# Optimization experiments

Hardware: AMD Instinct MI355X
Metric: run time of the kernel (lower is better)

## Reference

```python
import jax, jax.numpy as jnp
import numpy as np

N_NODES = 50000
N_EDGES = 800000
NUM_GRAPHS = 512
IN_DIM = 128
HID = 128
OUT_DIM = 1


def setup_inputs() -> dict:
    key = jax.random.key(0)
    ks = jax.random.split(key, 8)
    x = jax.random.normal(ks[0], (N_NODES, IN_DIM), dtype=jnp.float32)
    edge_index = jax.random.randint(ks[1], (2, N_EDGES), 0, N_NODES, dtype=jnp.int64)
    batch = jnp.sort(jax.random.randint(ks[2], (N_NODES,), 0, NUM_GRAPHS, dtype=jnp.int64))
    s1 = 1.0 / np.sqrt(IN_DIM)
    s2 = 1.0 / np.sqrt(HID)
    W1 = jax.random.normal(ks[3], (IN_DIM, HID), dtype=jnp.float32) * s1
    b1 = jnp.zeros((HID,), dtype=jnp.float32)
    W2 = jax.random.normal(ks[4], (HID, HID), dtype=jnp.float32) * s2
    b2 = jnp.zeros((HID,), dtype=jnp.float32)
    Wl = jax.random.normal(ks[5], (HID, OUT_DIM), dtype=jnp.float32) * s2
    bl = jnp.zeros((OUT_DIM,), dtype=jnp.float32)
    return {"x": x, "edge_index": edge_index, "batch": batch,
            "W1": W1, "b1": b1, "W2": W2, "b2": b2, "Wl": Wl, "bl": bl}


def _gcn_conv(x, src, dst, norm, W, b):
    # GCNConv: D^{-1/2}(A+I)D^{-1/2} X W + b (self-loops already in src/dst)
    h = x @ W                                    # [N, H]
    msg = h[src] * norm[:, None]                 # gather + edge-normalize
    agg = jax.ops.segment_sum(msg, dst, num_segments=N_NODES)  # scatter-add
    return agg + b


def reference(x, edge_index, batch, W1, b1, W2, b2, Wl, bl):
    loops = jnp.arange(N_NODES, dtype=edge_index.dtype)
    src = jnp.concatenate([edge_index[0], loops])
    dst = jnp.concatenate([edge_index[1], loops])
    deg = jax.ops.segment_sum(jnp.ones_like(dst, dtype=x.dtype), dst, num_segments=N_NODES)
    dinv = jax.lax.rsqrt(deg)                    # deg >= 1 due to self-loops
    norm = dinv[src] * dinv[dst]                 # symmetric normalization per edge

    h = jax.nn.relu(_gcn_conv(x, src, dst, norm, W1, b1))
    h = jax.nn.relu(_gcn_conv(h, src, dst, norm, W2, b2))

    # global_mean_pool over graph ids
    sums = jax.ops.segment_sum(h, batch, num_segments=NUM_GRAPHS)
    cnts = jax.ops.segment_sum(jnp.ones((N_NODES,), dtype=h.dtype), batch, num_segments=NUM_GRAPHS)
    pooled = sums / jnp.maximum(cnts, 1.0)[:, None]

    out = jax.nn.sigmoid(pooled @ Wl + bl)       # [G, 1]
    return out.squeeze(1)                        # [G]
```

## Files before the change

### kernel.cpp

```cpp
#include <hip/hip_runtime.h>
#include <hip/hip_bf16.h>

#define N_NODES 50000
#define N_EDGES 800000
#define NUM_GRAPHS 512
#define MAXDEG 64
#define EPB 4096
#define P1_BLOCKS 196
#define NBUCK 256
#define NPB 196

typedef short short8 __attribute__((ext_vector_type(8)));
typedef unsigned short u16x8 __attribute__((ext_vector_type(8)));
typedef float f32x4 __attribute__((ext_vector_type(4)));

__device__ __forceinline__ unsigned short f2bu(float f) {
    __hip_bfloat16 h = __float2bfloat16(f);
    return *reinterpret_cast<unsigned short*>(&h);
}
__device__ __forceinline__ float bu2f(unsigned short u) {
    unsigned int v = ((unsigned int)u) << 16;
    float f;
    __builtin_memcpy(&f, &v, 4);
    return f;
}

__global__ __launch_bounds__(256) void bin_k(const int* __restrict__ ei,
                                             unsigned int* __restrict__ staging,
                                             int* __restrict__ cnts_tbl,
                                             int* __restrict__ offs_tbl,
                                             unsigned short* __restrict__ hs1,
                                             unsigned short* __restrict__ hs2) {
    __shared__ unsigned int st[EPB];
    __shared__ int cnt[NBUCK], cur[NBUCK], scan[NBUCK];
    int b = blockIdx.x, t = threadIdx.x;
    if (b == 0 && t < 64)
        ((unsigned int*)(hs1 + (size_t)N_NODES * 128))[t] = 0u;
    if (b == 1 && t < 64)
        ((unsigned int*)(hs2 + (size_t)N_NODES * 128))[t] = 0u;
    cnt[t] = 0;
    __syncthreads();

    int e0 = b * EPB;
    int srcv[16], dstv[16], bk[16];
#pragma unroll
    for (int k = 0; k < 16; ++k) {
        int e = e0 + k * 256 + t;
        bool ok = e < N_EDGES;
        srcv[k] = ok ? ei[e] : 0;
        dstv[k] = ok ? ei[N_EDGES + e] : 0;
        bk[k] = ok ? (dstv[k] / NPB) : -1;
        if (ok) atomicAdd(&cnt[bk[k]], 1);
    }
    __syncthreads();
    scan[t] = cnt[t];
    __syncthreads();
    for (int off = 1; off < 256; off <<= 1) {
        int u = t >= off ? scan[t - off] : 0;
        __syncthreads();
        scan[t] += u;
        __syncthreads();
    }
    int excl = scan[t] - cnt[t];
    cur[t] = excl;
    cnts_tbl[t * P1_BLOCKS + b] = cnt[t];
    offs_tbl[t * P1_BLOCKS + b] = excl;
    __syncthreads();
#pragma unroll
    for (int k = 0; k < 16; ++k) {
        if (bk[k] >= 0) {
            int pos = atomicAdd(&cur[bk[k]], 1);
            int dl = dstv[k] - bk[k] * NPB;
            st[pos] = (unsigned int)srcv[k] | ((unsigned int)dl << 16);
        }
    }
    __syncthreads();
    unsigned int* gout = staging + (size_t)b * EPB;
    for (int i = t; i < EPB; i += 256) gout[i] = st[i];
}

__global__ __launch_bounds__(256) void adjbuild_k(const unsigned int* __restrict__ staging,
                                                  const int* __restrict__ cnts_tbl,
                                                  const int* __restrict__ offs_tbl,
                                                  unsigned short* __restrict__ adj,
                                                  int* __restrict__ cnt,
                                                  float* __restrict__ dinv,
                                                  const float* __restrict__ W1,
                                                  const float* __restrict__ W2,
                                                  unsigned short* __restrict__ W1t,
                                                  unsigned short* __restrict__ W2t) {
    int b = blockIdx.x, t = threadIdx.x;
    if (b >= NBUCK) {
        int wb = b - NBUCK;
        const float* W = wb < 64 ? W1 : W2;
        unsigned short* Wt = wb < 64 ? W1t : W2t;
        int idx = (wb & 63) * 256 + t;
        int k = idx >> 7, n = idx & 127;
        Wt[n * 128 + k] = f2bu(W[idx]);
        return;
    }
    __shared__ unsigned short adjL[NPB * MAXDEG];
    __shared__ int cntL[NPB];
    __shared__ int segStart[P1_BLOCKS + 1];
    __shared__ int segOff[P1_BLOCKS];
    __shared__ int tmp[256];

    if (t < NPB) cntL[t] = 0;
    int c = t < P1_BLOCKS ? cnts_tbl[b * P1_BLOCKS + t] : 0;
    if (t < P1_BLOCKS) segOff[t] = offs_tbl[b * P1_BLOCKS + t];
    tmp[t] = c;
    __syncthreads();
    for (int off = 1; off < 256; off <<= 1) {
        int u = t >= off ? tmp[t - off] : 0;
        __syncthreads();
        tmp[t] += u;
        __syncthreads();
    }
    if (t < P1_BLOCKS) segStart[t] = tmp[t] - c;
    if (t == 0) segStart[P1_BLOCKS] = tmp[P1_BLOCKS - 1];
    __syncthreads();

    int T = segStart[P1_BLOCKS];
    for (int f = t; f < T; f += 256) {
        int lo = 0, hi = P1_BLOCKS;
        while (hi - lo > 1) {
            int m = (lo + hi) >> 1;
            if (segStart[m] <= f) lo = m; else hi = m;
        }
        unsigned int p = staging[(size_t)lo * EPB + segOff[lo] + (f - segStart[lo])];
        int src = p & 0xFFFF;
        int dl = p >> 16;
        int slot = atomicAdd(&cntL[dl], 1);
        if (slot < MAXDEG - 1) adjL[dl * MAXDEG + slot] = (unsigned short)src;
    }
    __syncthreads();

    int nodeBase = b * NPB;
    if (t < NPB) {
        int node = nodeBase + t;
        int cc = cntL[t];
        int ec = cc < MAXDEG - 1 ? cc : MAXDEG - 1;
        adjL[t * MAXDEG + ec] = (unsigned short)node;
        int tot = ec + 1, tot4 = (tot + 3) & ~3;
        for (int s = tot; s < tot4; ++s) adjL[t * MAXDEG + s] = (unsigned short)N_NODES;
        if (node < N_NODES) {
            cnt[node] = cc;
            dinv[node] = rsqrtf((float)cc + 1.0f);
        }
    }
    __syncthreads();
    unsigned int* g = (unsigned int*)(adj + (size_t)nodeBase * MAXDEG);
    const unsigned int* l = (const unsigned int*)adjL;
    for (int i = t; i < NPB * MAXDEG / 2; i += 256) g[i] = l[i];
}

__global__ __launch_bounds__(256) void gemm_k(const float* __restrict__ Ap,
                                              const unsigned short* __restrict__ Wt,
                                              const float* __restrict__ dinv,
                                              unsigned short* __restrict__ C) {
    __shared__ unsigned short Wl[128 * 136];
    int t = threadIdx.x;
    for (int idx = t; idx < 2048; idx += 256) {
        int n = idx >> 4, c = idx & 15;
        *(u16x8*)(Wl + n * 136 + c * 8) = *(const u16x8*)(Wt + n * 128 + c * 8);
    }
    __syncthreads();

    int wave = t >> 6, lane = t & 63, quad = lane >> 4, ln = lane & 15;
    int rb = blockIdx.x * 128 + wave * 16;

    short8 a[2][4];
#pragma unroll
    for (int mt = 0; mt < 2; ++mt) {
        int r = rb + mt * 64 + ln;
        r = r < N_NODES ? r : N_NODES - 1;
        const float* arow = Ap + (size_t)r * 128 + quad * 8;
#pragma unroll
        for (int ks = 0; ks < 4; ++ks) {
            float4 v0 = *(const float4*)(arow + ks * 32);
            float4 v1 = *(const float4*)(arow + ks * 32 + 4);
            short8 av;
            av[0] = (short)f2bu(v0.x); av[1] = (short)f2bu(v0.y);
            av[2] = (short)f2bu(v0.z); av[3] = (short)f2bu(v0.w);
            av[4] = (short)f2bu(v1.x); av[5] = (short)f2bu(v1.y);
            av[6] = (short)f2bu(v1.z); av[7] = (short)f2bu(v1.w);
            a[mt][ks] = av;
        }
    }

    f32x4 acc[2][8];
#pragma unroll
    for (int mt = 0; mt < 2; ++mt)
#pragma unroll
        for (int ct = 0; ct < 8; ++ct) acc[mt][ct] = (f32x4){0.f, 0.f, 0.f, 0.f};

#pragma unroll
    for (int ks = 0; ks < 4; ++ks)
#pragma unroll
        for (int ct = 0; ct < 8; ++ct) {
            short8 b = *(const short8*)(Wl + (ct * 16 + ln) * 136 + ks * 32 + quad * 8);
            acc[0][ct] = __builtin_amdgcn_mfma_f32_16x16x32_bf16(a[0][ks], b, acc[0][ct], 0, 0, 0);
            acc[1][ct] = __builtin_amdgcn_mfma_f32_16x16x32_bf16(a[1][ks], b, acc[1][ct], 0, 0, 0);
        }

#pragma unroll
    for (int mt = 0; mt < 2; ++mt) {
#pragma unroll
        for (int rr = 0; rr < 4; ++rr) {
            int r = rb + mt * 64 + quad * 4 + rr;
            if (r >= N_NODES) continue;
            float dv = dinv[r];
#pragma unroll
            for (int ct = 0; ct < 8; ++ct)
                C[(size_t)r * 128 + ct * 16 + ln] = f2bu(acc[mt][ct][rr] * dv);
        }
    }
}

__global__ __launch_bounds__(256) void agg_gemm_k(const unsigned short* __restrict__ hs1,
                                                  const unsigned short* __restrict__ adj,
                                                  const int* __restrict__ cnt,
                                                  const float* __restrict__ dinv,
                                                  const float* __restrict__ bias,
                                                  const unsigned short* __restrict__ W2t,
                                                  unsigned short* __restrict__ hs2) {
    __shared__ unsigned short Wl[128 * 136];
    __shared__ unsigned short h1t[16 * 136];
    int t = threadIdx.x, wave = t >> 6, lane = t & 63;
    int quad = lane >> 4, fl = lane & 15;
    for (int idx = t; idx < 2048; idx += 256) {
        int n = idx >> 4, c = idx & 15;
        *(u16x8*)(Wl + n * 136 + c * 8) = *(const u16x8*)(W2t + n * 128 + c * 8);
    }
    int nb = blockIdx.x * 16;

    float4 b0 = *(const float4*)(bias + fl * 8);
    float4 b1f = *(const float4*)(bias + fl * 8 + 4);

#pragma unroll
    for (int q = 0; q < 4; ++q) {
        int lr = wave * 4 + q;
        int node = nb + lr;
        int idxv = (int)adj[node * MAXDEG + lane];
        int c = cnt[node];
        int ec = c < MAXDEG - 1 ? c : MAXDEG - 1;
        int iters = (ec + 4) >> 2;

        float acc[8];
#pragma unroll
        for (int j = 0; j < 8; ++j) acc[j] = 0.f;

        int i = 0;
        for (; i + 2 <= iters; i += 2) {
            int s0 = __shfl(idxv, i * 4 + quad, 64);
            int s1 = __shfl(idxv, i * 4 + 4 + quad, 64);
            u16x8 v0 = *(const u16x8*)(hs1 + (size_t)s0 * 128 + fl * 8);
            u16x8 v1 = *(const u16x8*)(hs1 + (size_t)s1 * 128 + fl * 8);
#pragma unroll
            for (int j = 0; j < 8; ++j) acc[j] += bu2f(v0[j]) + bu2f(v1[j]);
        }
        if (i < iters) {
            int s0 = __shfl(idxv, i * 4 + quad, 64);
            u16x8 v0 = *(const u16x8*)(hs1 + (size_t)s0 * 128 + fl * 8);
#pragma unroll
            for (int j = 0; j < 8; ++j) acc[j] += bu2f(v0[j]);
        }
#pragma unroll
        for (int j = 0; j < 8; ++j) {
            acc[j] += __shfl_xor(acc[j], 16, 64);
            acc[j] += __shfl_xor(acc[j], 32, 64);
        }
        if (quad == 0) {
            float dv = dinv[node];
            u16x8 o;
            o[0] = f2bu(fmaxf(acc[0] * dv + b0.x, 0.f));
            o[1] = f2bu(fmaxf(acc[1] * dv + b0.y, 0.f));
            o[2] = f2bu(fmaxf(acc[2] * dv + b0.z, 0.f));
            o[3] = f2bu(fmaxf(acc[3] * dv + b0.w, 0.f));
            o[4] = f2bu(fmaxf(acc[4] * dv + b1f.x, 0.f));
            o[5] = f2bu(fmaxf(acc[5] * dv + b1f.y, 0.f));
            o[6] = f2bu(fmaxf(acc[6] * dv + b1f.z, 0.f));
            o[7] = f2bu(fmaxf(acc[7] * dv + b1f.w, 0.f));
            *(u16x8*)(h1t + lr * 136 + fl * 8) = o;
        }
    }
    __syncthreads();

    int ln = fl;
    short8 a[4];
#pragma unroll
    for (int ks = 0; ks < 4; ++ks)
        a[ks] = *(const short8*)(h1t + ln * 136 + ks * 32 + quad * 8);

    f32x4 acc2[2];
    acc2[0] = (f32x4){0.f, 0.f, 0.f, 0.f};
    acc2[1] = (f32x4){0.f, 0.f, 0.f, 0.f};
#pragma unroll
    for (int ks = 0; ks < 4; ++ks)
#pragma unroll
        for (int ct = 0; ct < 2; ++ct) {
            short8 b = *(const short8*)(Wl + (wave * 32 + ct * 16 + ln) * 136 + ks * 32 + quad * 8);
            acc2[ct] = __builtin_amdgcn_mfma_f32_16x16x32_bf16(a[ks], b, acc2[ct], 0, 0, 0);
        }

    float dvr[4];
#pragma unroll
    for (int rr = 0; rr < 4; ++rr) dvr[rr] = dinv[nb + quad * 4 + rr];
#pragma unroll
    for (int ct = 0; ct < 2; ++ct)
#pragma unroll
        for (int rr = 0; rr < 4; ++rr) {
            int node = nb + quad * 4 + rr;
            hs2[(size_t)node * 128 + wave * 32 + ct * 16 + ln] = f2bu(acc2[ct][rr] * dvr[rr]);
        }
}

__global__ __launch_bounds__(256) void agg_k(const unsigned short* __restrict__ hs,
                                             const unsigned short* __restrict__ adj,
                                             const int* __restrict__ cnt,
                                             const float* __restrict__ dinv,
                                             const float* __restrict__ bias,
                                             unsigned short* __restrict__ out) {
    int wave = threadIdx.x >> 6, lane = threadIdx.x & 63;
    int node = blockIdx.x * 4 + wave;
    int quad = lane >> 4, fl = lane & 15;
    int idx = (int)adj[node * MAXDEG + lane];
    int c = cnt[node];
    int ec = c < MAXDEG - 1 ? c : MAXDEG - 1;
    int iters = (ec + 4) >> 2;

    float acc[8];
#pragma unroll
    for (int j = 0; j < 8; ++j) acc[j] = 0.f;

    int i = 0;
    for (; i + 2 <= iters; i += 2) {
        int s0 = __shfl(idx, i * 4 + quad, 64);
        int s1 = __shfl(idx, i * 4 + 4 + quad, 64);
        u16x8 v0 = *(const u16x8*)(hs + (size_t)s0 * 128 + fl * 8);
        u16x8 v1 = *(const u16x8*)(hs + (size_t)s1 * 128 + fl * 8);
#pragma unroll
        for (int j = 0; j < 8; ++j) acc[j] += bu2f(v0[j]) + bu2f(v1[j]);
    }
    if (i < iters) {
        int s0 = __shfl(idx, i * 4 + quad, 64);
        u16x8 v0 = *(const u16x8*)(hs + (size_t)s0 * 128 + fl * 8);
#pragma unroll
        for (int j = 0; j < 8; ++j) acc[j] += bu2f(v0[j]);
    }

#pragma unroll
    for (int j = 0; j < 8; ++j) {
        acc[j] += __shfl_xor(acc[j], 16, 64);
        acc[j] += __shfl_xor(acc[j], 32, 64);
    }

    if (quad == 0) {
        float dv = dinv[node];
        float4 b0 = *(const float4*)(bias + fl * 8);
        float4 b1 = *(const float4*)(bias + fl * 8 + 4);
        u16x8 o;
        o[0] = f2bu(fmaxf(acc[0] * dv + b0.x, 0.f));
        o[1] = f2bu(fmaxf(acc[1] * dv + b0.y, 0.f));
        o[2] = f2bu(fmaxf(acc[2] * dv + b0.z, 0.f));
        o[3] = f2bu(fmaxf(acc[3] * dv + b0.w, 0.f));
        o[4] = f2bu(fmaxf(acc[4] * dv + b1.x, 0.f));
        o[5] = f2bu(fmaxf(acc[5] * dv + b1.y, 0.f));
        o[6] = f2bu(fmaxf(acc[6] * dv + b1.z, 0.f));
        o[7] = f2bu(fmaxf(acc[7] * dv + b1.w, 0.f));
        *(u16x8*)(out + (size_t)node * 128 + fl * 8) = o;
    }
}

__device__ __forceinline__ int lb(const int* a, int n, int v) {
    int lo = 0, hi = n;
    while (lo < hi) {
        int m = (lo + hi) >> 1;
        if (a[m] < v) lo = m + 1;
        else hi = m;
    }
    return lo;
}

__global__ __launch_bounds__(256) void pool_k(const unsigned short* __restrict__ h2,
                                              const int* __restrict__ batch,
                                              const float* __restrict__ Wl,
                                              const float* __restrict__ bl,
                                              float* __restrict__ out) {
    __shared__ float buf[256];
    __shared__ float part[4];
    int g = blockIdx.x, t = threadIdx.x;
    int fp = t & 63, stripe = t >> 6;
    int lo = lb(batch, N_NODES, g), hi = lb(batch, N_NODES, g + 1);
    float s0 = 0.f, s1 = 0.f;
    for (int r = lo + stripe; r < hi; r += 4) {
        unsigned int u = *(const unsigned int*)(h2 + (size_t)r * 128 + fp * 2);
        s0 += bu2f((unsigned short)(u & 0xFFFF));
        s1 += bu2f((unsigned short)(u >> 16));
    }
    float p = s0 * Wl[fp * 2] + s1 * Wl[fp * 2 + 1];
#pragma unroll
    for (int o = 32; o > 0; o >>= 1) p += __shfl_down(p, o, 64);
    if ((t & 63) == 0) part[t >> 6] = p;
    __syncthreads();
    if (t == 0) {
        float cf = (float)(hi - lo);
        float z = (part[0] + part[1] + part[2] + part[3]) / fmaxf(cf, 1.f) + bl[0];
        out[g] = 1.f / (1.f + expf(-z));
    }
    (void)buf;
}

extern "C" void kernel_launch(void* const* d_in, const int* in_sizes, int n_in,
                              void* d_out, int out_size, void* d_ws, size_t ws_size,
                              hipStream_t stream) {
    const float* x = (const float*)d_in[0];
    const int* ei = (const int*)d_in[1];
    const int* batch = (const int*)d_in[2];
    const float* W1 = (const float*)d_in[3];
    const float* b1 = (const float*)d_in[4];
    const float* W2 = (const float*)d_in[5];
    const float* b2 = (const float*)d_in[6];
    const float* Wl = (const float*)d_in[7];
    const float* bl = (const float*)d_in[8];
    float* out = (float*)d_out;

    char* ws = (char*)d_ws;
    unsigned int* staging = (unsigned int*)(ws + 0x0);
    int* cnts_tbl = (int*)(ws + 0x310000);
    int* offs_tbl = (int*)(ws + 0x341000);
    unsigned short* adj = (unsigned short*)(ws + 0x372000);
    int* cnt = (int*)(ws + 0x992000);
    float* dinv = (float*)(ws + 0x9C3000);
    unsigned short* W1t = (unsigned short*)(ws + 0x9F4000);
    unsigned short* W2t = (unsigned short*)(ws + 0x9FC000);
    unsigned short* hs1 = (unsigned short*)(ws + 0xA04000);
    unsigned short* hs2 = (unsigned short*)(ws + 0x1640000);
    unsigned short* h2b = (unsigned short*)(ws + 0x2280000);

    bin_k<<<P1_BLOCKS, 256, 0, stream>>>(ei, staging, cnts_tbl, offs_tbl, hs1, hs2);
    adjbuild_k<<<NBUCK + 128, 256, 0, stream>>>(staging, cnts_tbl, offs_tbl,
                                                adj, cnt, dinv, W1, W2, W1t, W2t);

    gemm_k<<<(N_NODES + 127) / 128, 256, 0, stream>>>(x, W1t, dinv, hs1);
    agg_gemm_k<<<N_NODES / 16, 256, 0, stream>>>(hs1, adj, cnt, dinv, b1, W2t, hs2);
    agg_k<<<N_NODES / 4, 256, 0, stream>>>(hs2, adj, cnt, dinv, b2, h2b);

    pool_k<<<NUM_GRAPHS, 256, 0, stream>>>(h2b, batch, Wl, bl, out);
}
```

Measured before the change: 206.1 us.

## Fuse layer-2 aggregation with mean-pool projection; read W2 directly; unroll gathers

The second aggregation kernel now applies bias, ReLU and the final linear projection per node, reduces across lanes and atomically adds a scalar into a per-graph sum. This removes the bf16 write and re-read of the full layer-2 activation matrix and the pool kernel's scan over it. A small final kernel divides by node counts and applies the sigmoid. Separately, the aggregation loops are unrolled to four gathers per iteration, and agg_gemm_k reads W2t straight from global memory instead of staging it in LDS. The atomics add contention on 512 graph slots, and the fp32 summation order changes.

```diff
diff --git a/kernel.cpp b/kernel.cpp
--- a/kernel.cpp
+++ b/kernel.cpp
@@ -30,7 +30,8 @@
                                              int* __restrict__ cnts_tbl,
                                              int* __restrict__ offs_tbl,
                                              unsigned short* __restrict__ hs1,
-                                             unsigned short* __restrict__ hs2) {
+                                             unsigned short* __restrict__ hs2,
+                                             float* __restrict__ gsum) {
     __shared__ unsigned int st[EPB];
     __shared__ int cnt[NBUCK], cur[NBUCK], scan[NBUCK];
     int b = blockIdx.x, t = threadIdx.x;
@@ -38,6 +39,7 @@
         ((unsigned int*)(hs1 + (size_t)N_NODES * 128))[t] = 0u;
     if (b == 1 && t < 64)
         ((unsigned int*)(hs2 + (size_t)N_NODES * 128))[t] = 0u;
+    if (b == 2) { gsum[t] = 0.f; gsum[t + 256] = 0.f; }
     cnt[t] = 0;
     __syncthreads();
 
@@ -224,14 +226,9 @@
                                                   const float* __restrict__ bias,
                                                   const unsigned short* __restrict__ W2t,
                                                   unsigned short* __restrict__ hs2) {
-    __shared__ unsigned short Wl[128 * 136];
     __shared__ unsigned short h1t[16 * 136];
     int t = threadIdx.x, wave = t >> 6, lane = t & 63;
     int quad = lane >> 4, fl = lane & 15;
-    for (int idx = t; idx < 2048; idx += 256) {
-        int n = idx >> 4, c = idx & 15;
-        *(u16x8*)(Wl + n * 136 + c * 8) = *(const u16x8*)(W2t + n * 128 + c * 8);
-    }
     int nb = blockIdx.x * 16;
 
     float4 b0 = *(const float4*)(bias + fl * 8);
@@ -251,15 +248,20 @@
         for (int j = 0; j < 8; ++j) acc[j] = 0.f;
 
         int i = 0;
-        for (; i + 2 <= iters; i += 2) {
+        for (; i + 4 <= iters; i += 4) {
             int s0 = __shfl(idxv, i * 4 + quad, 64);
             int s1 = __shfl(idxv, i * 4 + 4 + quad, 64);
+            int s2 = __shfl(idxv, i * 4 + 8 + quad, 64);
+            int s3 = __shfl(idxv, i * 4 + 12 + quad, 64);
             u16x8 v0 = *(const u16x8*)(hs1 + (size_t)s0 * 128 + fl * 8);
             u16x8 v1 = *(const u16x8*)(hs1 + (size_t)s1 * 128 + fl * 8);
-#pragma unroll
-            for (int j = 0; j < 8; ++j) acc[j] += bu2f(v0[j]) + bu2f(v1[j]);
-        }
-        if (i < iters) {
+            u16x8 v2 = *(const u16x8*)(hs1 + (size_t)s2 * 128 + fl * 8);
+            u16x8 v3 = *(const u16x8*)(hs1 + (size_t)s3 * 128 + fl * 8);
+#pragma unroll
+            for (int j = 0; j < 8; ++j)
+                acc[j] += (bu2f(v0[j]) + bu2f(v1[j])) + (bu2f(v2[j]) + bu2f(v3[j]));
+        }
+        for (; i < iters; ++i) {
             int s0 = __shfl(idxv, i * 4 + quad, 64);
             u16x8 v0 = *(const u16x8*)(hs1 + (size_t)s0 * 128 + fl * 8);
 #pragma unroll
@@ -299,7 +301,7 @@
     for (int ks = 0; ks < 4; ++ks)
 #pragma unroll
         for (int ct = 0; ct < 2; ++ct) {
-            short8 b = *(const short8*)(Wl + (wave * 32 + ct * 16 + ln) * 136 + ks * 32 + quad * 8);
+            short8 b = *(const short8*)(W2t + (wave * 32 + ct * 16 + ln) * 128 + ks * 32 + quad * 8);
             acc2[ct] = __builtin_amdgcn_mfma_f32_16x16x32_bf16(a[ks], b, acc2[ct], 0, 0, 0);
         }
 
@@ -315,12 +317,14 @@
         }
 }
 
-__global__ __launch_bounds__(256) void agg_k(const unsigned short* __restrict__ hs,
-                                             const unsigned short* __restrict__ adj,
-                                             const int* __restrict__ cnt,
-                                             const float* __restrict__ dinv,
-                                             const float* __restrict__ bias,
-                                             unsigned short* __restrict__ out) {
+__global__ __launch_bounds__(256) void agg_pool_k(const unsigned short* __restrict__ hs,
+                                                  const unsigned short* __restrict__ adj,
+                                                  const int* __restrict__ cnt,
+                                                  const float* __restrict__ dinv,
+                                                  const float* __restrict__ bias,
+                                                  const float* __restrict__ Wl,
+                                                  const int* __restrict__ batch,
+                                                  float* __restrict__ gsum) {
     int wave = threadIdx.x >> 6, lane = threadIdx.x & 63;
     int node = blockIdx.x * 4 + wave;
     int quad = lane >> 4, fl = lane & 15;
@@ -334,15 +338,20 @@
     for (int j = 0; j < 8; ++j) acc[j] = 0.f;
 
     int i = 0;
-    for (; i + 2 <= iters; i += 2) {
+    for (; i + 4 <= iters; i += 4) {
         int s0 = __shfl(idx, i * 4 + quad, 64);
         int s1 = __shfl(idx, i * 4 + 4 + quad, 64);
+        int s2 = __shfl(idx, i * 4 + 8 + quad, 64);
+        int s3 = __shfl(idx, i * 4 + 12 + quad, 64);
         u16x8 v0 = *(const u16x8*)(hs + (size_t)s0 * 128 + fl * 8);
         u16x8 v1 = *(const u16x8*)(hs + (size_t)s1 * 128 + fl * 8);
-#pragma unroll
-        for (int j = 0; j < 8; ++j) acc[j] += bu2f(v0[j]) + bu2f(v1[j]);
-    }
-    if (i < iters) {
+        u16x8 v2 = *(const u16x8*)(hs + (size_t)s2 * 128 + fl * 8);
+        u16x8 v3 = *(const u16x8*)(hs + (size_t)s3 * 128 + fl * 8);
+#pragma unroll
+        for (int j = 0; j < 8; ++j)
+            acc[j] += (bu2f(v0[j]) + bu2f(v1[j])) + (bu2f(v2[j]) + bu2f(v3[j]));
+    }
+    for (; i < iters; ++i) {
         int s0 = __shfl(idx, i * 4 + quad, 64);
         u16x8 v0 = *(const u16x8*)(hs + (size_t)s0 * 128 + fl * 8);
 #pragma unroll
@@ -359,16 +368,21 @@
         float dv = dinv[node];
         float4 b0 = *(const float4*)(bias + fl * 8);
         float4 b1 = *(const float4*)(bias + fl * 8 + 4);
-        u16x8 o;
-        o[0] = f2bu(fmaxf(acc[0] * dv + b0.x, 0.f));
-        o[1] = f2bu(fmaxf(acc[1] * dv + b0.y, 0.f));
-        o[2] = f2bu(fmaxf(acc[2] * dv + b0.z, 0.f));
-        o[3] = f2bu(fmaxf(acc[3] * dv + b0.w, 0.f));
-        o[4] = f2bu(fmaxf(acc[4] * dv + b1.x, 0.f));
-        o[5] = f2bu(fmaxf(acc[5] * dv + b1.y, 0.f));
-        o[6] = f2bu(fmaxf(acc[6] * dv + b1.z, 0.f));
-        o[7] = f2bu(fmaxf(acc[7] * dv + b1.w, 0.f));
-        *(u16x8*)(out + (size_t)node * 128 + fl * 8) = o;
+        float4 w0 = *(const float4*)(Wl + fl * 8);
+        float4 w1 = *(const float4*)(Wl + fl * 8 + 4);
+        float p = fmaxf(acc[0] * dv + b0.x, 0.f) * w0.x
+                + fmaxf(acc[1] * dv + b0.y, 0.f) * w0.y
+                + fmaxf(acc[2] * dv + b0.z, 0.f) * w0.z
+                + fmaxf(acc[3] * dv + b0.w, 0.f) * w0.w
+                + fmaxf(acc[4] * dv + b1.x, 0.f) * w1.x
+                + fmaxf(acc[5] * dv + b1.y, 0.f) * w1.y
+                + fmaxf(acc[6] * dv + b1.z, 0.f) * w1.z
+                + fmaxf(acc[7] * dv + b1.w, 0.f) * w1.w;
+        p += __shfl_xor(p, 1, 64);
+        p += __shfl_xor(p, 2, 64);
+        p += __shfl_xor(p, 4, 64);
+        p += __shfl_xor(p, 8, 64);
+        if (fl == 0) atomicAdd(&gsum[batch[node]], p);
     }
 }
 
@@ -382,33 +396,16 @@
     return lo;
 }
 
-__global__ __launch_bounds__(256) void pool_k(const unsigned short* __restrict__ h2,
-                                              const int* __restrict__ batch,
-                                              const float* __restrict__ Wl,
-                                              const float* __restrict__ bl,
-                                              float* __restrict__ out) {
-    __shared__ float buf[256];
-    __shared__ float part[4];
-    int g = blockIdx.x, t = threadIdx.x;
-    int fp = t & 63, stripe = t >> 6;
+__global__ __launch_bounds__(256) void final_k(const float* __restrict__ gsum,
+                                               const int* __restrict__ batch,
+                                               const float* __restrict__ bl,
+                                               float* __restrict__ out) {
+    int g = blockIdx.x * 256 + threadIdx.x;
+    if (g >= NUM_GRAPHS) return;
     int lo = lb(batch, N_NODES, g), hi = lb(batch, N_NODES, g + 1);
-    float s0 = 0.f, s1 = 0.f;
-    for (int r = lo + stripe; r < hi; r += 4) {
-        unsigned int u = *(const unsigned int*)(h2 + (size_t)r * 128 + fp * 2);
-        s0 += bu2f((unsigned short)(u & 0xFFFF));
-        s1 += bu2f((unsigned short)(u >> 16));
-    }
-    float p = s0 * Wl[fp * 2] + s1 * Wl[fp * 2 + 1];
-#pragma unroll
-    for (int o = 32; o > 0; o >>= 1) p += __shfl_down(p, o, 64);
-    if ((t & 63) == 0) part[t >> 6] = p;
-    __syncthreads();
-    if (t == 0) {
-        float cf = (float)(hi - lo);
-        float z = (part[0] + part[1] + part[2] + part[3]) / fmaxf(cf, 1.f) + bl[0];
-        out[g] = 1.f / (1.f + expf(-z));
-    }
-    (void)buf;
+    float cf = (float)(hi - lo);
+    float z = gsum[g] / fmaxf(cf, 1.f) + bl[0];
+    out[g] = 1.f / (1.f + expf(-z));
 }
 
 extern "C" void kernel_launch(void* const* d_in, const int* in_sizes, int n_in,
@@ -434,17 +431,17 @@
     float* dinv = (float*)(ws + 0x9C3000);
     unsigned short* W1t = (unsigned short*)(ws + 0x9F4000);
     unsigned short* W2t = (unsigned short*)(ws + 0x9FC000);
+    float* gsum = (float*)(ws + 0xA02000);
     unsigned short* hs1 = (unsigned short*)(ws + 0xA04000);
     unsigned short* hs2 = (unsigned short*)(ws + 0x1640000);
-    unsigned short* h2b = (unsigned short*)(ws + 0x2280000);
-
-    bin_k<<<P1_BLOCKS, 256, 0, stream>>>(ei, staging, cnts_tbl, offs_tbl, hs1, hs2);
+
+    bin_k<<<P1_BLOCKS, 256, 0, stream>>>(ei, staging, cnts_tbl, offs_tbl, hs1, hs2, gsum);
     adjbuild_k<<<NBUCK + 128, 256, 0, stream>>>(staging, cnts_tbl, offs_tbl,
                                                 adj, cnt, dinv, W1, W2, W1t, W2t);
 
     gemm_k<<<(N_NODES + 127) / 128, 256, 0, stream>>>(x, W1t, dinv, hs1);
     agg_gemm_k<<<N_NODES / 16, 256, 0, stream>>>(hs1, adj, cnt, dinv, b1, W2t, hs2);
-    agg_k<<<N_NODES / 4, 256, 0, stream>>>(hs2, adj, cnt, dinv, b2, h2b);
-
-    pool_k<<<NUM_GRAPHS, 256, 0, stream>>>(h2b, batch, Wl, bl, out);
-}
+    agg_pool_k<<<N_NODES / 4, 256, 0, stream>>>(hs2, adj, cnt, dinv, b2, Wl, batch, gsum);
+
+    final_k<<<(NUM_GRAPHS + 255) / 256, 256, 0, stream>>>(gsum, batch, bl, out);
+}
```

After: 272.8 us. +32.4%, slower.
